# Kernel optimization log

Hardware: AMD Instinct MI355X
Metric: run time of the kernel (lower is better)

## Reference

```python
import jax, jax.numpy as jnp
import numpy as np

E, H, B, S = 512, 8, 8, 1024  # embed_dim, n_head, batch, n_agent (sequence)
DH = E // H
DECAY_SCALING = 1.0


def _rmsnorm(x, scale, eps=1e-6):
    return x * jax.lax.rsqrt(jnp.mean(x * x, axis=-1, keepdims=True) + eps) * scale


def _groupnorm(y, scale, bias, n_head, eps=1e-5):
    # GroupNorm with num_groups = n_head over the feature axis (flax semantics).
    b, s, e = y.shape
    yg = y.reshape(b, s, n_head, e // n_head)
    mu = jnp.mean(yg, axis=-1, keepdims=True)
    var = jnp.var(yg, axis=-1, keepdims=True)
    yn = (yg - mu) * jax.lax.rsqrt(var + eps)
    return yn.reshape(b, s, e) * scale + bias


def _decay_kappas(n_head, scaling):
    # RetNet multi-scale decays: 1 - exp(linspace(log(1/32), log(1/512), H))
    k = 1.0 - jnp.exp(jnp.linspace(jnp.log(1.0 / 32.0), jnp.log(1.0 / 512.0), n_head))
    return (k * scaling).astype(jnp.float32)


def _msr(key_x, query_x, value_x, wq, wk, wv, wg, wo, gs, gb, kappas):
    # Parallel multi-scale retention (masked / causal, full_self_retention=False).
    b, s, e = query_x.shape
    h = wq.shape[0]
    q = jnp.einsum('bse,hed->bhsd', query_x, wq)
    k = jnp.einsum('bse,hed->bhsd', key_x, wk)
    v = jnp.einsum('bse,hed->bhsd', value_x, wv)
    n = jnp.arange(s)
    diff = n[:, None] - n[None, :]
    causal = diff >= 0
    expnt = jnp.where(causal, diff, 0).astype(q.dtype)
    # D[h,n,m] = kappa_h^(n-m) for n>=m else 0
    D = jnp.where(causal[None], kappas[:, None, None] ** expnt[None], 0.0)
    scores = jnp.einsum('bhnd,bhmd->bhnm', q, k) * D[None]  # [B,H,S,S]
    ret = jnp.einsum('bhnm,bhmd->bhnd', scores, v)
    ret = ret.transpose(0, 2, 1, 3).reshape(b, s, e)
    ret = _groupnorm(ret, gs, gb, h)
    return (jax.nn.swish(query_x @ wg) * ret) @ wo


def _swiglu(x, w_gate, w_lin, w_out):
    return (jax.nn.swish(x @ w_gate) * (x @ w_lin)) @ w_out


def setup_inputs() -> dict:
    key = jax.random.key(0)
    ks = jax.random.split(key, 20)
    sc = 0.02
    d = {
        'x': jax.random.normal(ks[0], (B, S, E), jnp.float32),
        'obs_rep': jax.random.normal(ks[1], (B, S, E), jnp.float32),
        # retention 1 params
        'wq1': jax.random.normal(ks[2], (H, E, DH), jnp.float32) * sc,
        'wk1': jax.random.normal(ks[3], (H, E, DH), jnp.float32) * sc,
        'wv1': jax.random.normal(ks[4], (H, E, DH), jnp.float32) * sc,
        'wg1': jax.random.normal(ks[5], (E, E), jnp.float32) * sc,
        'wo1': jax.random.normal(ks[6], (E, E), jnp.float32) * sc,
        'gs1': jnp.ones((E,), jnp.float32),
        'gb1': jnp.zeros((E,), jnp.float32),
        # retention 2 params
        'wq2': jax.random.normal(ks[7], (H, E, DH), jnp.float32) * sc,
        'wk2': jax.random.normal(ks[8], (H, E, DH), jnp.float32) * sc,
        'wv2': jax.random.normal(ks[9], (H, E, DH), jnp.float32) * sc,
        'wg2': jax.random.normal(ks[10], (E, E), jnp.float32) * sc,
        'wo2': jax.random.normal(ks[11], (E, E), jnp.float32) * sc,
        'gs2': jnp.ones((E,), jnp.float32),
        'gb2': jnp.zeros((E,), jnp.float32),
        # RMSNorm scales
        'ln1_s': jnp.ones((E,), jnp.float32),
        'ln2_s': jnp.ones((E,), jnp.float32),
        'ln3_s': jnp.ones((E,), jnp.float32),
        # SwiGLU(hidden=E, input=E)
        'ffn_w_lin': jax.random.normal(ks[12], (E, E), jnp.float32) * sc,
        'ffn_w_gate': jax.random.normal(ks[13], (E, E), jnp.float32) * sc,
        'ffn_w_out': jax.random.normal(ks[14], (E, E), jnp.float32) * sc,
    }
    return d


def reference(x, obs_rep, wq1, wk1, wv1, wg1, wo1, gs1, gb1,
              wq2, wk2, wv2, wg2, wo2, gs2, gb2,
              ln1_s, ln2_s, ln3_s, ffn_w_lin, ffn_w_gate, ffn_w_out):
    kappas = _decay_kappas(H, DECAY_SCALING)
    # x = ln1(x + retn1(key=x, query=x, value=x))
    x1 = _rmsnorm(x + _msr(x, x, x, wq1, wk1, wv1, wg1, wo1, gs1, gb1, kappas), ln1_s)
    # x = ln2(obs_rep + retn2(key=x1, query=obs_rep, value=x1))
    x2 = _rmsnorm(obs_rep + _msr(x1, obs_rep, x1, wq2, wk2, wv2, wg2, wo2, gs2, gb2, kappas), ln2_s)
    # out = ln3(x2 + ffn(x2))
    return _rmsnorm(x2 + _swiglu(x2, ffn_w_gate, ffn_w_lin, ffn_w_out), ln3_s)
```

## Files before the change

### kernel.cpp

```cpp
#include <hip/hip_runtime.h>
#include <hip/hip_bf16.h>
#include <stdint.h>

typedef unsigned short u16;
typedef unsigned int   u32;
typedef __bf16 bf16x8 __attribute__((ext_vector_type(8)));
typedef u16    u16x8  __attribute__((ext_vector_type(8)));
typedef float  f32x4  __attribute__((ext_vector_type(4)));

#define E_   512
#define H_   8
#define DH_  64
#define B_   8
#define S_   1024
#define M_   (B_ * S_)
#define NTOT (M_ * E_)

__device__ __forceinline__ u16 f2bf(float f) {
    u32 x = __float_as_uint(f);
    x += 0x7fffu + ((x >> 16) & 1u);
    return (u16)(x >> 16);
}
__device__ __forceinline__ float bf2f(u16 b) { return __uint_as_float((u32)b << 16); }
__device__ __forceinline__ bf16x8 as_bf(u16x8 v) {
    union { u16x8 u; bf16x8 b; } x; x.u = v; return x.b;
}
__device__ __forceinline__ u32 cvtpk(float lo, float hi) {
    u32 r;
    asm("v_cvt_pk_bf16_f32 %0, %1, %2" : "=v"(r) : "v"(lo), "v"(hi));
    return r;
}
__device__ __forceinline__ void gll16(const u16* g, u16* l) {
    __builtin_amdgcn_global_load_lds((const __attribute__((address_space(1))) u32*)g,
                                     (__attribute__((address_space(3))) u32*)l, 16, 0, 0);
}
__device__ __forceinline__ void xcd_map(int f, int nwg, int gx, int& bx, int& by) {
    int nf = (f & 7) * (nwg >> 3) + (f >> 3);
    bx = nf % gx; by = nf / gx;
}

__global__ __launch_bounds__(256) void prep_weights(
    const float* __restrict__ wq1, const float* __restrict__ wk1, const float* __restrict__ wv1,
    const float* __restrict__ wg1, const float* __restrict__ wq2, const float* __restrict__ wk2,
    const float* __restrict__ wv2, const float* __restrict__ wg2, const float* __restrict__ wgat,
    const float* __restrict__ wlin, const float* __restrict__ wo1, const float* __restrict__ wo2,
    const float* __restrict__ wout,
    u16* __restrict__ WC1, u16* __restrict__ WC2, u16* __restrict__ WF,
    u16* __restrict__ WO1t, u16* __restrict__ WO2t, u16* __restrict__ WOUt) {
    __shared__ float tle[64][65];
    const int rt = blockIdx.y, c0 = blockIdx.x * 64, tid = threadIdx.x;
    u16* dst; const float* src; int lr0; bool qkv = false; int nb0 = 0, h = 0;
    if (rt < 64) {
        bool s1 = rt < 32;
        dst = s1 ? WC1 : WC2;
        int r = (rt & 31) * 64; lr0 = r;
        if (r < 1536) {
            qkv = true; h = (r >> 6) & 7;
            src = (r < 512) ? (s1 ? wq1 : wq2) : (r < 1024) ? (s1 ? wk1 : wk2) : (s1 ? wv1 : wv2);
        } else { src = s1 ? wg1 : wg2; nb0 = r - 1536; }
    } else if (rt < 80) {
        dst = WF; int r = (rt - 64) * 64; lr0 = r;
        src = (r < 512) ? wgat : wlin; nb0 = r & 511;
    } else if (rt < 88) { dst = WO1t; lr0 = (rt - 80) * 64; src = wo1; nb0 = lr0; }
    else if (rt < 96)   { dst = WO2t; lr0 = (rt - 88) * 64; src = wo2; nb0 = lr0; }
    else                { dst = WOUt; lr0 = (rt - 96) * 64; src = wout; nb0 = lr0; }

    #pragma unroll
    for (int i = 0; i < 16; ++i) {
        int idx = i * 256 + tid, a = idx >> 6, b = idx & 63;
        tle[a][b] = qkv ? src[(size_t)(h * 512 + c0 + a) * 64 + b]
                        : src[(size_t)(c0 + a) * 512 + nb0 + b];
    }
    __syncthreads();
    #pragma unroll
    for (int i = 0; i < 16; ++i) {
        int idx = i * 256 + tid;
        dst[(size_t)(lr0 + (idx >> 6)) * 512 + c0 + (idx & 63)] = f2bf(tle[idx & 63][idx >> 6]);
    }
}

__global__ __launch_bounds__(256) void cvt_both(const float* __restrict__ x,
                                                const float* __restrict__ obs,
                                                u16* __restrict__ XB, u16* __restrict__ OB) {
    int i = blockIdx.x * 256 + threadIdx.x;
    float4 v = ((const float4*)x)[i];
    ushort4 o;
    o.x = f2bf(v.x); o.y = f2bf(v.y); o.z = f2bf(v.z); o.w = f2bf(v.w);
    ((ushort4*)XB)[i] = o;
    v = ((const float4*)obs)[i];
    o.x = f2bf(v.x); o.y = f2bf(v.y); o.z = f2bf(v.z); o.w = f2bf(v.w);
    ((ushort4*)OB)[i] = o;
}

__global__ __launch_bounds__(256) void gemm_qkvg(const u16* __restrict__ A1,
                                                 const u16* __restrict__ A2,
                                                 const u16* __restrict__ W,
                                                 u16* __restrict__ QB, u16* __restrict__ KB,
                                                 u16* __restrict__ KT, u16* __restrict__ VT,
                                                 u16* __restrict__ GB) {
    __shared__ u16 sh[32768];
    const int tid = threadIdx.x;
    const int l = tid & 63, w = tid >> 6;
    const int wm = w & 1, wn = w >> 1;
    int bx, by; xcd_map(blockIdx.x, 1024, 16, bx, by);
    const int bm = by * 128, bn = bx * 128;
    const int which = bx >> 2;
    const u16* A = (which == 1 || which == 2) ? A2 : A1;

    size_t srcA[4], srcB[4]; int ldst[4];
    #pragma unroll
    for (int c = 0; c < 4; ++c) {
        int row = c * 32 + w * 8 + (l >> 3);
        int chs = (l & 7) ^ (row & 7);
        srcA[c] = (size_t)(bm + row) * E_ + chs * 8;
        srcB[c] = (size_t)(bn + row) * E_ + chs * 8;
        ldst[c] = c * 2048 + w * 512;
    }
    int aoff[2][4], boff[2][4];
    #pragma unroll
    for (int kk = 0; kk < 2; ++kk)
        #pragma unroll
        for (int f = 0; f < 4; ++f) {
            int ra = wm * 64 + f * 16 + (l & 15);
            int rb = wn * 64 + f * 16 + (l & 15);
            int ch = kk * 4 + (l >> 4);
            aoff[kk][f] = ra * 128 + ((ch ^ (ra & 7)) << 4);
            boff[kk][f] = rb * 128 + ((ch ^ (rb & 7)) << 4);
        }

    f32x4 acc[4][4] = {};
    #pragma unroll
    for (int c = 0; c < 4; ++c) {
        gll16(A + srcA[c], &sh[ldst[c]]);
        gll16(W + srcB[c], &sh[16384 + ldst[c]]);
    }

    for (int t = 0; t < 8; ++t) {
        const int cur = t & 1;
        if (t < 7) {
            const int k1 = (t + 1) * 64;
            const int nb = (cur ^ 1) * 8192;
            #pragma unroll
            for (int c = 0; c < 4; ++c) {
                gll16(A + srcA[c] + k1, &sh[nb + ldst[c]]);
                gll16(W + srcB[c] + k1, &sh[16384 + nb + ldst[c]]);
            }
            asm volatile("s_waitcnt vmcnt(8)" ::: "memory");
        } else {
            asm volatile("s_waitcnt vmcnt(0)" ::: "memory");
        }
        __builtin_amdgcn_sched_barrier(0);
        __builtin_amdgcn_s_barrier();

        const char* ab = (const char*)sh + cur * 16384;
        const char* bb = (const char*)sh + 32768 + cur * 16384;
        #pragma unroll
        for (int kk = 0; kk < 2; ++kk) {
            bf16x8 af[4], bfr[4];
            #pragma unroll
            for (int f = 0; f < 4; ++f) {
                af[f]  = as_bf(*(const u16x8*)(ab + aoff[kk][f]));
                bfr[f] = as_bf(*(const u16x8*)(bb + boff[kk][f]));
            }
            __builtin_amdgcn_s_setprio(1);
            #pragma unroll
            for (int m = 0; m < 4; ++m)
                #pragma unroll
                for (int n = 0; n < 4; ++n)
                    acc[m][n] = __builtin_amdgcn_mfma_f32_16x16x32_bf16(af[m], bfr[n], acc[m][n], 0, 0, 0);
            __builtin_amdgcn_s_setprio(0);
        }
        if (t < 7) {
            __builtin_amdgcn_s_barrier();
            __builtin_amdgcn_sched_barrier(0);
        }
    }

    if (which != 2) {
        u16* dst = (which == 0) ? QB : (which == 1) ? KB : GB;
        #pragma unroll
        for (int m = 0; m < 4; ++m) {
            int row = bm + wm * 64 + m * 16 + ((l >> 4) << 2);
            #pragma unroll
            for (int n = 0; n < 4; ++n) {
                int coll = (bn & 511) + wn * 64 + n * 16 + (l & 15);
                f32x4 v = acc[m][n];
                #pragma unroll
                for (int r = 0; r < 4; ++r) dst[(size_t)(row + r) * E_ + coll] = f2bf(v[r]);
            }
        }
    }
    if (which == 1 || which == 2) {
        u16* dstT = (which == 2) ? VT : KT;
        __syncthreads();
        #pragma unroll
        for (int m = 0; m < 4; ++m) {
            int row0 = wm * 64 + m * 16 + ((l >> 4) << 2);
            #pragma unroll
            for (int n = 0; n < 4; ++n) {
                int c = wn * 64 + n * 16 + (l & 15);
                f32x4 v = acc[m][n];
                uint2 pk; pk.x = cvtpk(v[0], v[1]); pk.y = cvtpk(v[2], v[3]);
                int off = c * 256 + (((row0 >> 3) ^ (c & 7)) << 4) + ((row0 & 7) << 1);
                *(uint2*)((char*)sh + off) = pk;
            }
        }
        __syncthreads();
        int c = tid >> 1, half = tid & 1;
        int collg = (bn & 511) + c;
        int bh = ((bm >> 10) << 3) + (collg >> 6);
        size_t gb = ((size_t)bh * 64 + (collg & 63)) * 1024 + (bm & 1023) + half * 64;
        #pragma unroll
        for (int j = 0; j < 8; ++j) {
            int chunk = half * 8 + j;
            uint4 vv = *(const uint4*)((const char*)sh + c * 256 + ((chunk ^ (c & 7)) << 4));
            *(uint4*)(dstT + gb + j * 8) = vv;
        }
    }
}

__global__ __launch_bounds__(256) void state_u(const u16* __restrict__ KT,
                                               const u16* __restrict__ VT,
                                               u16* __restrict__ U) {
    const int id = blockIdx.x;
    const int bh = id >> 3, c = id & 7;
    const int h = bh & 7;
    const int l = threadIdx.x & 63, w = threadIdx.x >> 6;
    const float kappa = 1.0f - __expf(-3.46573590f + (float)h * -0.39608410f);
    const float log2k = log2f(kappa);
    const float ik = 1.0f / kappa;

    bf16x8 af[4];
    {
        size_t vbase = ((size_t)bh * 64 + (w * 16 + (l & 15))) * 1024 + c * 128 + ((l >> 4) << 3);
        #pragma unroll
        for (int kk = 0; kk < 4; ++kk)
            af[kk] = as_bf(*(const u16x8*)(VT + vbase + kk * 32));
    }

    f32x4 acc[4] = {};
    #pragma unroll
    for (int fd = 0; fd < 4; ++fd) {
        size_t kbase = ((size_t)bh * 64 + (fd * 16 + (l & 15))) * 1024 + c * 128 + ((l >> 4) << 3);
        #pragma unroll
        for (int kk = 0; kk < 4; ++kk) {
            u16x8 kv = *(const u16x8*)(KT + kbase + kk * 32);
            int mb = kk * 32 + ((l >> 4) << 3);
            float wj = exp2f((float)(127 - mb) * log2k);
            u16x8 kw;
            #pragma unroll
            for (int j = 0; j < 8; ++j) { kw[j] = f2bf(bf2f(kv[j]) * wj); wj *= ik; }
            acc[fd] = __builtin_amdgcn_mfma_f32_16x16x32_bf16(af[kk], as_bf(kw), acc[fd], 0, 0, 0);
        }
    }

    #pragma unroll
    for (int fd = 0; fd < 4; ++fd) {
        int dv = w * 16 + ((l >> 4) << 2);
        int dk = fd * 16 + (l & 15);
        size_t ub = ((size_t)id * 64 + dv) * 64 + dk;
        #pragma unroll
        for (int r = 0; r < 4; ++r) U[ub + (size_t)r * 64] = f2bf(acc[fd][r]);
    }
}

__global__ __launch_bounds__(256) void retention_chunk(
        const u16* __restrict__ Q, const u16* __restrict__ K,
        const u16* __restrict__ VT, const u16* __restrict__ U,
        const u16* __restrict__ G,
        const float* __restrict__ gs, const float* __restrict__ gb,
        u16* __restrict__ T) {
    __shared__ u16 Ks[128 * 64], Vts[64 * 128], Ps[128 * 64], Ss[64 * 64];
    const int tid = threadIdx.x;
    const int l = tid & 63, w = tid >> 6;
    const int id = blockIdx.x;
    const int bh = id >> 3, c = id & 7;
    const int h = bh & 7;
    const int n0 = c * 128;
    const size_t base = (size_t)(bh >> 3) * (S_ * E_) + h * DH_;

    const float kappa = 1.0f - __expf(-3.46573590f + (float)h * -0.39608410f);
    const float log2k = log2f(kappa);
    const float ik = 1.0f / kappa;
    const float ikp2 = ik * ik, ikp3 = ikp2 * ik;

    float gsv[4], gbv[4];
    #pragma unroll
    for (int fd = 0; fd < 4; ++fd) {
        gsv[fd] = gs[h * 64 + fd * 16 + (l & 15)];
        gbv[fd] = gb[h * 64 + fd * 16 + (l & 15)];
    }

    #pragma unroll
    for (int cc = 0; cc < 4; ++cc) {
        int row = cc * 32 + w * 8 + (l >> 3);
        int chs = (l & 7) ^ (row & 7);
        gll16(K + base + (size_t)(n0 + row) * E_ + chs * 8, &Ks[cc * 2048 + w * 512]);
        int d = cc * 16 + w * 4 + (l >> 4);
        int vch = (l & 15) ^ (d & 15);
        gll16(VT + ((size_t)bh * 64 + d) * 1024 + n0 + vch * 8, &Vts[cc * 2048 + w * 512]);
    }

    bf16x8 qf[2][2];
    #pragma unroll
    for (int kk = 0; kk < 2; ++kk)
        #pragma unroll
        for (int fn = 0; fn < 2; ++fn) {
            int n = n0 + fn * 64 + w * 16 + (l & 15);
            qf[kk][fn] = as_bf(*(const u16x8*)(Q + base + (size_t)n * E_ + kk * 32 + ((l >> 4) << 3)));
        }

    if (c > 0) {
        float accs[16];
        #pragma unroll
        for (int j = 0; j < 16; ++j) accs[j] = 0.f;
        const float kC = exp2f(128.0f * log2k);
        float wc = 1.0f;
        size_t ub = (size_t)bh * (8 * 4096) + tid * 16;
        for (int cp = c - 1; cp >= 0; --cp) {
            const u16* up = U + ub + (size_t)cp * 4096;
            u16x8 a = *(const u16x8*)up;
            u16x8 b = *(const u16x8*)(up + 8);
            #pragma unroll
            for (int j = 0; j < 8; ++j) {
                accs[j]     += bf2f(a[j]) * wc;
                accs[8 + j] += bf2f(b[j]) * wc;
            }
            wc *= kC;
        }
        int dv = tid >> 2, ch0 = (tid & 3) << 1;
        #pragma unroll
        for (int hh = 0; hh < 2; ++hh) {
            uint4 pk;
            pk.x = cvtpk(accs[hh * 8 + 0], accs[hh * 8 + 1]);
            pk.y = cvtpk(accs[hh * 8 + 2], accs[hh * 8 + 3]);
            pk.z = cvtpk(accs[hh * 8 + 4], accs[hh * 8 + 5]);
            pk.w = cvtpk(accs[hh * 8 + 6], accs[hh * 8 + 7]);
            *(uint4*)((char*)Ss + dv * 128 + (((ch0 + hh) ^ (dv & 7)) << 4)) = pk;
        }
    }
    __syncthreads();

    f32x4 acc[2][4] = {};

    if (c > 0) {
        __builtin_amdgcn_s_setprio(1);
        #pragma unroll
        for (int kk = 0; kk < 2; ++kk) {
            bf16x8 sf[4];
            #pragma unroll
            for (int fd = 0; fd < 4; ++fd) {
                int dv = fd * 16 + (l & 15);
                int ch = kk * 4 + (l >> 4);
                sf[fd] = as_bf(*(const u16x8*)((const char*)Ss + dv * 128 + ((ch ^ (dv & 7)) << 4)));
            }
            #pragma unroll
            for (int fn = 0; fn < 2; ++fn)
                #pragma unroll
                for (int fd = 0; fd < 4; ++fd)
                    acc[fn][fd] = __builtin_amdgcn_mfma_f32_16x16x32_bf16(qf[kk][fn], sf[fd], acc[fn][fd], 0, 0, 0);
        }
        __builtin_amdgcn_s_setprio(0);
        #pragma unroll
        for (int fn = 0; fn < 2; ++fn) {
            int nl0 = fn * 64 + w * 16 + ((l >> 4) << 2);
            float fr0 = exp2f((float)(nl0 + 1) * log2k);
            float fr1 = fr0 * kappa, fr2 = fr1 * kappa, fr3 = fr2 * kappa;
            #pragma unroll
            for (int fd = 0; fd < 4; ++fd) {
                acc[fn][fd][0] *= fr0; acc[fn][fd][1] *= fr1;
                acc[fn][fd][2] *= fr2; acc[fn][fd][3] *= fr3;
            }
        }
    }

    #pragma unroll
    for (int mh = 0; mh < 2; ++mh) {
        const int m0l = mh * 64;
        bf16x8 kf[2][4];
        #pragma unroll
        for (int kk = 0; kk < 2; ++kk)
            #pragma unroll
            for (int f = 0; f < 4; ++f) {
                int row = m0l + f * 16 + (l & 15);
                int ch = kk * 4 + (l >> 4);
                kf[kk][f] = as_bf(*(const u16x8*)((const char*)Ks + row * 128 + ((ch ^ (row & 7)) << 4)));
            }
        #pragma unroll
        for (int fn = 0; fn < 2; ++fn) {
            if (mh == 1 && fn == 0) continue;
            f32x4 s[4] = {};
            __builtin_amdgcn_s_setprio(1);
            #pragma unroll
            for (int kk = 0; kk < 2; ++kk)
                #pragma unroll
                for (int f = 0; f < 4; ++f)
                    s[f] = __builtin_amdgcn_mfma_f32_16x16x32_bf16(kf[kk][f], qf[kk][fn], s[f], 0, 0, 0);
            __builtin_amdgcn_s_setprio(0);
            const bool fast = (mh == 0 && fn == 1);
            int nl = fn * 64 + w * 16 + (l & 15);
            #pragma unroll
            for (int f = 0; f < 4; ++f) {
                int mbl = m0l + f * 16 + ((l >> 4) << 2);
                int delta = nl - mbl;
                float wb = exp2f((float)delta * log2k);
                f32x4 v = s[f];
                float p0, p1, p2, p3;
                if (fast) {
                    float w1 = wb * ik, w2 = w1 * ik, w3 = w2 * ik;
                    p0 = v[0] * wb; p1 = v[1] * w1; p2 = v[2] * w2; p3 = v[3] * w3;
                } else {
                    p0 = (delta >= 0) ? v[0] * wb : 0.f;
                    p1 = (delta >= 1) ? v[1] * wb * ik : 0.f;
                    p2 = (delta >= 2) ? v[2] * wb * ikp2 : 0.f;
                    p3 = (delta >= 3) ? v[3] * wb * ikp3 : 0.f;
                }
                int mcl = f * 16 + ((l >> 4) << 2);
                int byteoff = nl * 128 + (((mcl >> 3) ^ (nl & 7)) << 4) + ((mcl & 4) << 1);
                uint2 pk;
                pk.x = cvtpk(p0, p1);
                pk.y = cvtpk(p2, p3);
                *(uint2*)((char*)Ps + byteoff) = pk;
            }
        }
        #pragma unroll
        for (int km = 0; km < 2; ++km) {
            bf16x8 pf[2];
            #pragma unroll
            for (int fn = 0; fn < 2; ++fn) {
                if (mh == 1 && fn == 0) continue;
                int row = fn * 64 + w * 16 + (l & 15);
                int ch = km * 4 + (l >> 4);
                pf[fn] = as_bf(*(const u16x8*)((const char*)Ps + row * 128 + ((ch ^ (row & 7)) << 4)));
            }
            __builtin_amdgcn_s_setprio(1);
            #pragma unroll
            for (int fd = 0; fd < 4; ++fd) {
                int d = fd * 16 + (l & 15);
                int mch = mh * 8 + km * 4 + (l >> 4);
                bf16x8 vfr = as_bf(*(const u16x8*)((const char*)Vts + d * 256 + ((mch ^ (d & 15)) << 4)));
                #pragma unroll
                for (int fn = 0; fn < 2; ++fn) {
                    if (mh == 1 && fn == 0) continue;
                    acc[fn][fd] = __builtin_amdgcn_mfma_f32_16x16x32_bf16(pf[fn], vfr, acc[fn][fd], 0, 0, 0);
                }
            }
            __builtin_amdgcn_s_setprio(0);
        }
    }

    #pragma unroll
    for (int fn = 0; fn < 2; ++fn) {
        #pragma unroll
        for (int r = 0; r < 4; ++r) {
            float s1 = 0.f, s2 = 0.f;
            #pragma unroll
            for (int fd = 0; fd < 4; ++fd) { float v = acc[fn][fd][r]; s1 += v; s2 += v * v; }
            #pragma unroll
            for (int off = 1; off < 16; off <<= 1) {
                s1 += __shfl_xor(s1, off, 64);
                s2 += __shfl_xor(s2, off, 64);
            }
            float mean = s1 * (1.f / 64.f);
            float var  = s2 * (1.f / 64.f) - mean * mean;
            float rinv = rsqrtf(var + 1e-5f);
            int rowg = n0 + fn * 64 + w * 16 + ((l >> 4) << 2) + r;
            size_t rb = base + (size_t)rowg * E_;
            #pragma unroll
            for (int fd = 0; fd < 4; ++fd) {
                int d = fd * 16 + (l & 15);
                float ny = (acc[fn][fd][r] - mean) * rinv;
                float rn = ny * gsv[fd] + gbv[fd];
                float g = bf2f(G[rb + d]);
                T[rb + d] = f2bf(g * rn / (1.f + __expf(-g)));
            }
        }
    }
}

__global__ __launch_bounds__(256) void gemm_wo(const u16* __restrict__ A,
                                               const u16* __restrict__ W,
                                               u16* __restrict__ Cb) {
    __shared__ u16 Als[64 * 64];
    __shared__ u16 Bls[128 * 64];
    const int tid = threadIdx.x;
    const int l = tid & 63, w = tid >> 6;
    const int wm = w & 1, wn = w >> 1;
    int bx, by; xcd_map(blockIdx.x, 512, 4, bx, by);
    const int bm = by * 64, bn = bx * 128;

    size_t srcA[2], srcB[4]; int ldstA[2], ldstB[4];
    #pragma unroll
    for (int c = 0; c < 4; ++c) {
        int row = c * 32 + w * 8 + (l >> 3);
        int chs = (l & 7) ^ (row & 7);
        if (c < 2) { srcA[c] = (size_t)(bm + row) * E_ + chs * 8; ldstA[c] = c * 2048 + w * 512; }
        srcB[c] = (size_t)(bn + row) * E_ + chs * 8;
        ldstB[c] = c * 2048 + w * 512;
    }
    int aoff[2][2], boff[2][4];
    #pragma unroll
    for (int kk = 0; kk < 2; ++kk) {
        #pragma unroll
        for (int f = 0; f < 2; ++f) {
            int ra = wm * 32 + f * 16 + (l & 15);
            aoff[kk][f] = ra * 128 + (((kk * 4 + (l >> 4)) ^ (ra & 7)) << 4);
        }
        #pragma unroll
        for (int f = 0; f < 4; ++f) {
            int rb = wn * 64 + f * 16 + (l & 15);
            boff[kk][f] = rb * 128 + (((kk * 4 + (l >> 4)) ^ (rb & 7)) << 4);
        }
    }

    f32x4 acc[2][4] = {};
    for (int t = 0; t < 8; ++t) {
        const int k1 = t * 64;
        #pragma unroll
        for (int c = 0; c < 2; ++c) gll16(A + srcA[c] + k1, &Als[ldstA[c]]);
        #pragma unroll
        for (int c = 0; c < 4; ++c) gll16(W + srcB[c] + k1, &Bls[ldstB[c]]);
        __syncthreads();
        #pragma unroll
        for (int kk = 0; kk < 2; ++kk) {
            bf16x8 af[2], bfr[4];
            #pragma unroll
            for (int f = 0; f < 2; ++f) af[f] = as_bf(*(const u16x8*)((const char*)Als + aoff[kk][f]));
            #pragma unroll
            for (int f = 0; f < 4; ++f) bfr[f] = as_bf(*(const u16x8*)((const char*)Bls + boff[kk][f]));
            #pragma unroll
            for (int m = 0; m < 2; ++m)
                #pragma unroll
                for (int n = 0; n < 4; ++n)
                    acc[m][n] = __builtin_amdgcn_mfma_f32_16x16x32_bf16(af[m], bfr[n], acc[m][n], 0, 0, 0);
        }
        __syncthreads();
    }

    #pragma unroll
    for (int m = 0; m < 2; ++m) {
        int row = bm + wm * 32 + m * 16 + ((l >> 4) << 2);
        #pragma unroll
        for (int n = 0; n < 4; ++n) {
            int col = bn + wn * 64 + n * 16 + (l & 15);
            f32x4 v = acc[m][n];
            #pragma unroll
            for (int r = 0; r < 4; ++r) Cb[(size_t)(row + r) * E_ + col] = f2bf(v[r]);
        }
    }
}

__global__ __launch_bounds__(256) void gemm_ffn(const u16* __restrict__ A,
                                                const u16* __restrict__ W,
                                                u16* __restrict__ T) {
    __shared__ u16 Als[64 * 64];
    __shared__ u16 Bgs[64 * 64];
    __shared__ u16 Bls[64 * 64];
    const int tid = threadIdx.x;
    const int l = tid & 63, w = tid >> 6;
    const int wm = w & 1, wn = w >> 1;
    int bx, by; xcd_map(blockIdx.x, 1024, 8, bx, by);
    const int bm = by * 64, bn = bx * 64;

    size_t srcA[2], srcG[2], srcL[2]; int ldst[2];
    #pragma unroll
    for (int c = 0; c < 2; ++c) {
        int row = c * 32 + w * 8 + (l >> 3);
        int chs = (l & 7) ^ (row & 7);
        srcA[c] = (size_t)(bm + row) * E_ + chs * 8;
        srcG[c] = (size_t)(bn + row) * E_ + chs * 8;
        srcL[c] = (size_t)(512 + bn + row) * E_ + chs * 8;
        ldst[c] = c * 2048 + w * 512;
    }
    int aoff[2][2], goff[2][2];
    #pragma unroll
    for (int kk = 0; kk < 2; ++kk)
        #pragma unroll
        for (int f = 0; f < 2; ++f) {
            int ra = wm * 32 + f * 16 + (l & 15);
            int rb = wn * 32 + f * 16 + (l & 15);
            aoff[kk][f] = ra * 128 + (((kk * 4 + (l >> 4)) ^ (ra & 7)) << 4);
            goff[kk][f] = rb * 128 + (((kk * 4 + (l >> 4)) ^ (rb & 7)) << 4);
        }

    f32x4 accg[2][2] = {}, accl[2][2] = {};
    for (int t = 0; t < 8; ++t) {
        const int k1 = t * 64;
        #pragma unroll
        for (int c = 0; c < 2; ++c) {
            gll16(A + srcA[c] + k1, &Als[ldst[c]]);
            gll16(W + srcG[c] + k1, &Bgs[ldst[c]]);
            gll16(W + srcL[c] + k1, &Bls[ldst[c]]);
        }
        __syncthreads();
        #pragma unroll
        for (int kk = 0; kk < 2; ++kk) {
            bf16x8 af[2], bg[2], bl[2];
            #pragma unroll
            for (int f = 0; f < 2; ++f) {
                af[f] = as_bf(*(const u16x8*)((const char*)Als + aoff[kk][f]));
                bg[f] = as_bf(*(const u16x8*)((const char*)Bgs + goff[kk][f]));
                bl[f] = as_bf(*(const u16x8*)((const char*)Bls + goff[kk][f]));
            }
            #pragma unroll
            for (int m = 0; m < 2; ++m)
                #pragma unroll
                for (int n = 0; n < 2; ++n) {
                    accg[m][n] = __builtin_amdgcn_mfma_f32_16x16x32_bf16(af[m], bg[n], accg[m][n], 0, 0, 0);
                    accl[m][n] = __builtin_amdgcn_mfma_f32_16x16x32_bf16(af[m], bl[n], accl[m][n], 0, 0, 0);
                }
        }
        __syncthreads();
    }

    #pragma unroll
    for (int m = 0; m < 2; ++m) {
        int row = bm + wm * 32 + m * 16 + ((l >> 4) << 2);
        #pragma unroll
        for (int n = 0; n < 2; ++n) {
            int col = bn + wn * 32 + n * 16 + (l & 15);
            #pragma unroll
            for (int r = 0; r < 4; ++r) {
                float g = accg[m][n][r], lv = accl[m][n][r];
                T[(size_t)(row + r) * E_ + col] = f2bf(g * lv / (1.f + __expf(-g)));
            }
        }
    }
}

__global__ __launch_bounds__(256) void rmsnorm_res(const u16* __restrict__ Xb,
                                                   const u16* __restrict__ Yb,
                                                   const float* __restrict__ sc,
                                                   float* __restrict__ outf,
                                                   u16* __restrict__ outb) {
    int row = blockIdx.x * 4 + (threadIdx.x >> 6);
    int l = threadIdx.x & 63;
    size_t off = (size_t)row * E_ + l * 8;
    u16x8 xv = *(const u16x8*)(Xb + off);
    u16x8 yv = *(const u16x8*)(Yb + off);
    float v[8]; float sq = 0.f;
    #pragma unroll
    for (int j = 0; j < 8; ++j) { v[j] = bf2f(xv[j]) + bf2f(yv[j]); sq += v[j] * v[j]; }
    #pragma unroll
    for (int o = 1; o < 64; o <<= 1) sq += __shfl_xor(sq, o, 64);
    float rinv = rsqrtf(sq * (1.0f / 512.0f) + 1e-6f);
    float4 s0 = ((const float4*)sc)[l * 2];
    float4 s1 = ((const float4*)sc)[l * 2 + 1];
    float sv[8] = {s0.x, s0.y, s0.z, s0.w, s1.x, s1.y, s1.z, s1.w};
    if (outb) {
        u16x8 o8;
        #pragma unroll
        for (int j = 0; j < 8; ++j) o8[j] = f2bf(v[j] * rinv * sv[j]);
        *(u16x8*)(outb + off) = o8;
    }
    if (outf) {
        float4 o0, o1;
        o0.x = v[0]*rinv*sv[0]; o0.y = v[1]*rinv*sv[1]; o0.z = v[2]*rinv*sv[2]; o0.w = v[3]*rinv*sv[3];
        o1.x = v[4]*rinv*sv[4]; o1.y = v[5]*rinv*sv[5]; o1.z = v[6]*rinv*sv[6]; o1.w = v[7]*rinv*sv[7];
        ((float4*)(outf))[(off >> 2)]     = o0;
        ((float4*)(outf))[(off >> 2) + 1] = o1;
    }
}

extern "C" void kernel_launch(void* const* d_in, const int* in_sizes, int n_in,
                              void* d_out, int out_size, void* d_ws, size_t ws_size,
                              hipStream_t stream) {
    const float* x    = (const float*)d_in[0];
    const float* obs  = (const float*)d_in[1];
    const float* wq1  = (const float*)d_in[2];
    const float* wk1  = (const float*)d_in[3];
    const float* wv1  = (const float*)d_in[4];
    const float* wg1  = (const float*)d_in[5];
    const float* wo1  = (const float*)d_in[6];
    const float* gs1  = (const float*)d_in[7];
    const float* gb1  = (const float*)d_in[8];
    const float* wq2  = (const float*)d_in[9];
    const float* wk2  = (const float*)d_in[10];
    const float* wv2  = (const float*)d_in[11];
    const float* wg2  = (const float*)d_in[12];
    const float* wo2  = (const float*)d_in[13];
    const float* gs2  = (const float*)d_in[14];
    const float* gb2  = (const float*)d_in[15];
    const float* ln1s = (const float*)d_in[16];
    const float* ln2s = (const float*)d_in[17];
    const float* ln3s = (const float*)d_in[18];
    const float* wlin = (const float*)d_in[19];
    const float* wgat = (const float*)d_in[20];
    const float* wout = (const float*)d_in[21];

    u16* wsb = (u16*)d_ws;
    u16* WC1  = wsb;
    u16* WC2  = WC1 + 2048 * 512;
    u16* WF   = WC2 + 2048 * 512;
    u16* WO1t = WF + 1024 * 512;
    u16* WO2t = WO1t + 512 * 512;
    u16* WOUt = WO2t + 512 * 512;
    u16* XB   = WOUt + 512 * 512;
    u16* OB   = XB + NTOT;
    u16* QB   = OB + NTOT;
    u16* KB   = QB + NTOT;
    u16* KT   = KB + NTOT;
    u16* VT   = KT + NTOT;
    u16* GB   = VT + NTOT;
    u16* TB   = GB + NTOT;
    u16* UB   = TB + NTOT;
    u16* YB   = QB;

    dim3 tG(256);

    prep_weights<<<dim3(8, 104), tG, 0, stream>>>(wq1, wk1, wv1, wg1, wq2, wk2, wv2, wg2,
                                                  wgat, wlin, wo1, wo2, wout,
                                                  WC1, WC2, WF, WO1t, WO2t, WOUt);
    cvt_both<<<NTOT / 1024, tG, 0, stream>>>(x, obs, XB, OB);

    gemm_qkvg<<<1024, tG, 0, stream>>>(XB, XB, WC1, QB, KB, KT, VT, GB);
    state_u<<<512, tG, 0, stream>>>(KT, VT, UB);
    retention_chunk<<<512, tG, 0, stream>>>(QB, KB, VT, UB, GB, gs1, gb1, TB);
    gemm_wo<<<512, tG, 0, stream>>>(TB, WO1t, YB);
    rmsnorm_res<<<M_ / 4, tG, 0, stream>>>(XB, YB, ln1s, nullptr, XB);

    gemm_qkvg<<<1024, tG, 0, stream>>>(OB, XB, WC2, QB, KB, KT, VT, GB);
    state_u<<<512, tG, 0, stream>>>(KT, VT, UB);
    retention_chunk<<<512, tG, 0, stream>>>(QB, KB, VT, UB, GB, gs2, gb2, TB);
    gemm_wo<<<512, tG, 0, stream>>>(TB, WO2t, YB);
    rmsnorm_res<<<M_ / 4, tG, 0, stream>>>(OB, YB, ln2s, nullptr, OB);

    gemm_ffn<<<1024, tG, 0, stream>>>(OB, WF, TB);
    gemm_wo<<<512, tG, 0, stream>>>(TB, WOUt, YB);
    rmsnorm_res<<<M_ / 4, tG, 0, stream>>>(OB, YB, ln3s, (float*)d_out, nullptr);
}
```

Before: 172.9 us.

## Double-buffer LDS loads in output and FFN GEMMs with prefetch and raised MFMA priority

Converts the Wo projection GEMM and the fused SwiGLU FFN GEMM from single-buffered LDS tiles to a two-stage ping-pong buffer. The next K tile's global-to-LDS loads are issued before the current tile's MFMAs, and a partial vmcnt wait is used so memory latency overlaps compute. It also raises wave priority around the MFMA block. This doubles LDS use per block (48 KB), which may reduce occupancy, and relies on hand-placed waitcnt and barrier ordering being correct.

```diff
diff --git a/kernel.cpp b/kernel.cpp
--- a/kernel.cpp
+++ b/kernel.cpp
@@ -481,8 +481,7 @@
 __global__ __launch_bounds__(256) void gemm_wo(const u16* __restrict__ A,
                                                const u16* __restrict__ W,
                                                u16* __restrict__ Cb) {
-    __shared__ u16 Als[64 * 64];
-    __shared__ u16 Bls[128 * 64];
+    __shared__ u16 sh[24576];
     const int tid = threadIdx.x;
     const int l = tid & 63, w = tid >> 6;
     const int wm = w & 1, wn = w >> 1;
@@ -514,27 +513,48 @@
     }
 
     f32x4 acc[2][4] = {};
+    #pragma unroll
+    for (int c = 0; c < 2; ++c) gll16(A + srcA[c], &sh[ldstA[c]]);
+    #pragma unroll
+    for (int c = 0; c < 4; ++c) gll16(W + srcB[c], &sh[8192 + ldstB[c]]);
+
     for (int t = 0; t < 8; ++t) {
-        const int k1 = t * 64;
-        #pragma unroll
-        for (int c = 0; c < 2; ++c) gll16(A + srcA[c] + k1, &Als[ldstA[c]]);
-        #pragma unroll
-        for (int c = 0; c < 4; ++c) gll16(W + srcB[c] + k1, &Bls[ldstB[c]]);
-        __syncthreads();
+        const int cur = t & 1;
+        if (t < 7) {
+            const int k1 = (t + 1) * 64;
+            const int na = (cur ^ 1) * 4096, nb = (cur ^ 1) * 8192;
+            #pragma unroll
+            for (int c = 0; c < 2; ++c) gll16(A + srcA[c] + k1, &sh[na + ldstA[c]]);
+            #pragma unroll
+            for (int c = 0; c < 4; ++c) gll16(W + srcB[c] + k1, &sh[8192 + nb + ldstB[c]]);
+            asm volatile("s_waitcnt vmcnt(6)" ::: "memory");
+        } else {
+            asm volatile("s_waitcnt vmcnt(0)" ::: "memory");
+        }
+        __builtin_amdgcn_sched_barrier(0);
+        __builtin_amdgcn_s_barrier();
+
+        const char* ab = (const char*)sh + cur * 8192;
+        const char* bb = (const char*)sh + 16384 + cur * 16384;
         #pragma unroll
         for (int kk = 0; kk < 2; ++kk) {
             bf16x8 af[2], bfr[4];
             #pragma unroll
-            for (int f = 0; f < 2; ++f) af[f] = as_bf(*(const u16x8*)((const char*)Als + aoff[kk][f]));
-            #pragma unroll
-            for (int f = 0; f < 4; ++f) bfr[f] = as_bf(*(const u16x8*)((const char*)Bls + boff[kk][f]));
+            for (int f = 0; f < 2; ++f) af[f] = as_bf(*(const u16x8*)(ab + aoff[kk][f]));
+            #pragma unroll
+            for (int f = 0; f < 4; ++f) bfr[f] = as_bf(*(const u16x8*)(bb + boff[kk][f]));
+            __builtin_amdgcn_s_setprio(1);
             #pragma unroll
             for (int m = 0; m < 2; ++m)
                 #pragma unroll
                 for (int n = 0; n < 4; ++n)
                     acc[m][n] = __builtin_amdgcn_mfma_f32_16x16x32_bf16(af[m], bfr[n], acc[m][n], 0, 0, 0);
-        }
-        __syncthreads();
+            __builtin_amdgcn_s_setprio(0);
+        }
+        if (t < 7) {
+            __builtin_amdgcn_s_barrier();
+            __builtin_amdgcn_sched_barrier(0);
+        }
     }
 
     #pragma unroll
@@ -553,9 +573,7 @@
 __global__ __launch_bounds__(256) void gemm_ffn(const u16* __restrict__ A,
                                                 const u16* __restrict__ W,
                                                 u16* __restrict__ T) {
-    __shared__ u16 Als[64 * 64];
-    __shared__ u16 Bgs[64 * 64];
-    __shared__ u16 Bls[64 * 64];
+    __shared__ u16 sh[24576];
     const int tid = threadIdx.x;
     const int l = tid & 63, w = tid >> 6;
     const int wm = w & 1, wn = w >> 1;
@@ -584,24 +602,44 @@
         }
 
     f32x4 accg[2][2] = {}, accl[2][2] = {};
+    #pragma unroll
+    for (int c = 0; c < 2; ++c) {
+        gll16(A + srcA[c], &sh[ldst[c]]);
+        gll16(W + srcG[c], &sh[8192 + ldst[c]]);
+        gll16(W + srcL[c], &sh[16384 + ldst[c]]);
+    }
+
     for (int t = 0; t < 8; ++t) {
-        const int k1 = t * 64;
-        #pragma unroll
-        for (int c = 0; c < 2; ++c) {
-            gll16(A + srcA[c] + k1, &Als[ldst[c]]);
-            gll16(W + srcG[c] + k1, &Bgs[ldst[c]]);
-            gll16(W + srcL[c] + k1, &Bls[ldst[c]]);
-        }
-        __syncthreads();
+        const int cur = t & 1;
+        if (t < 7) {
+            const int k1 = (t + 1) * 64;
+            const int nb = (cur ^ 1) * 4096;
+            #pragma unroll
+            for (int c = 0; c < 2; ++c) {
+                gll16(A + srcA[c] + k1, &sh[nb + ldst[c]]);
+                gll16(W + srcG[c] + k1, &sh[8192 + nb + ldst[c]]);
+                gll16(W + srcL[c] + k1, &sh[16384 + nb + ldst[c]]);
+            }
+            asm volatile("s_waitcnt vmcnt(6)" ::: "memory");
+        } else {
+            asm volatile("s_waitcnt vmcnt(0)" ::: "memory");
+        }
+        __builtin_amdgcn_sched_barrier(0);
+        __builtin_amdgcn_s_barrier();
+
+        const char* ab = (const char*)sh + cur * 8192;
+        const char* gb = (const char*)sh + 16384 + cur * 8192;
+        const char* lb = (const char*)sh + 32768 + cur * 8192;
         #pragma unroll
         for (int kk = 0; kk < 2; ++kk) {
             bf16x8 af[2], bg[2], bl[2];
             #pragma unroll
             for (int f = 0; f < 2; ++f) {
-                af[f] = as_bf(*(const u16x8*)((const char*)Als + aoff[kk][f]));
-                bg[f] = as_bf(*(const u16x8*)((const char*)Bgs + goff[kk][f]));
-                bl[f] = as_bf(*(const u16x8*)((const char*)Bls + goff[kk][f]));
-            }
+                af[f] = as_bf(*(const u16x8*)(ab + aoff[kk][f]));
+                bg[f] = as_bf(*(const u16x8*)(gb + goff[kk][f]));
+                bl[f] = as_bf(*(const u16x8*)(lb + goff[kk][f]));
+            }
+            __builtin_amdgcn_s_setprio(1);
             #pragma unroll
             for (int m = 0; m < 2; ++m)
                 #pragma unroll
@@ -609,8 +647,12 @@
                     accg[m][n] = __builtin_amdgcn_mfma_f32_16x16x32_bf16(af[m], bg[n], accg[m][n], 0, 0, 0);
                     accl[m][n] = __builtin_amdgcn_mfma_f32_16x16x32_bf16(af[m], bl[n], accl[m][n], 0, 0, 0);
                 }
-        }
-        __syncthreads();
+            __builtin_amdgcn_s_setprio(0);
+        }
+        if (t < 7) {
+            __builtin_amdgcn_s_barrier();
+            __builtin_amdgcn_sched_barrier(0);
+        }
     }
 
     #pragma unroll
```

Result: no change. 170.9 us (-1.1%).
